# Kernel tuning notes

Measured on AMD Instinct MI355X. Metric: run time of the kernel, lower is better.

The kernel has to match this reference:

```python
import jax, jax.numpy as jnp
from jax import lax
import numpy as np

N = 2000      # num_nodes
T_IN = 24
T_OUT = 12
B = 32
H = 64        # hidden_dim
D = 10        # embed_dim / adapt_dim
K = 2         # cheb_k
C_IN = 1


def setup_inputs() -> dict:
    key = jax.random.key(0)
    ks = jax.random.split(key, 13)
    s = 0.1  # xavier-ish scale
    f32 = jnp.float32
    return {
        "x": jax.random.normal(ks[0], (B, T_IN, N), f32),
        "node_emb": jax.random.normal(ks[1], (N, D), f32) * s,
        "adapt_emb": jax.random.normal(ks[2], (N, D), f32) * s,
        # layer 0 NAPL weight/bias pools (gate: 2H out, candidate: H out)
        "Wg0": jax.random.normal(ks[3], (D, K, C_IN + H, 2 * H), f32) * s,
        "bg0": jax.random.normal(ks[4], (D, 2 * H), f32) * s,
        "Wc0": jax.random.normal(ks[5], (D, K, C_IN + H, H), f32) * s,
        "bc0": jax.random.normal(ks[6], (D, H), f32) * s,
        # layer 1 pools (input is hidden_dim)
        "Wg1": jax.random.normal(ks[7], (D, K, 2 * H, 2 * H), f32) * s,
        "bg1": jax.random.normal(ks[8], (D, 2 * H), f32) * s,
        "Wc1": jax.random.normal(ks[9], (D, K, 2 * H, H), f32) * s,
        "bc1": jax.random.normal(ks[10], (D, H), f32) * s,
        # 1x1 conv head == per-node linear hidden -> T_out
        "head_w": jax.random.normal(ks[11], (T_OUT, H), f32) * s,
        "head_b": jnp.zeros((T_OUT,), f32),
    }


def reference(x, node_emb, adapt_emb, Wg0, bg0, Wc0, bc0, Wg1, bg1, Wc1, bc1,
              head_w, head_b):
    Bn, T, Nn = x.shape
    # adaptive adjacency: row-softmax(relu(E E^T)); no prior -> A_used = A_adapt
    A = jax.nn.softmax(jax.nn.relu(adapt_emb @ adapt_emb.T), axis=-1)
    supports = jnp.stack([jnp.eye(Nn, dtype=x.dtype), A])  # (K, N, N)

    def napl(Wp, bp):
        # node-adaptive parameter learning: per-node weights/biases
        W = jnp.einsum('nd,dkio->nkio', node_emb, Wp)  # (N, K, Cin, Cout)
        b = node_emb @ bp                              # (N, Cout)
        return W, b

    p = [napl(Wg0, bg0), napl(Wc0, bc0), napl(Wg1, bg1), napl(Wc1, bc1)]

    def gconv(inp, W, b):
        # inp: (B, N, C)
        xg = jnp.einsum('knm,bmc->bknc', supports, inp)      # (B, K, N, C)
        return jnp.einsum('bkni,nkio->bno', xg, W) + b       # (B, N, Cout)

    def cell(xt, h, gW, gb, cW, cb):
        zr = jax.nn.sigmoid(gconv(jnp.concatenate([xt, h], -1), gW, gb))
        z, r = jnp.split(zr, 2, axis=-1)
        hc = jnp.tanh(gconv(jnp.concatenate([xt, r * h], -1), cW, cb))
        return z * h + (1.0 - z) * hc

    def step(carry, xt):
        h0, h1 = carry
        h0 = cell(xt, h0, p[0][0], p[0][1], p[1][0], p[1][1])
        h1 = cell(h0, h1, p[2][0], p[2][1], p[3][0], p[3][1])
        return (h0, h1), None

    xs = jnp.transpose(x[..., None], (1, 0, 2, 3))  # (T, B, N, 1)
    h0 = jnp.zeros((Bn, Nn, H), x.dtype)
    h1 = jnp.zeros((Bn, Nn, H), x.dtype)
    (h0, h1), _ = lax.scan(step, (h0, h1), xs)

    # 1x1 conv head on (B, H, N, 1) == per-node linear: (B, T_out, N)
    y = jnp.einsum('bnh,oh->bon', h1, head_w) + head_b[None, :, None]
    return y
```

## Files before the change

kernel.cpp:

```cpp
#include <hip/hip_runtime.h>
#include <math.h>

#define NN 2000
#define BB 32
#define TT 24
#define T_OUT 12
#define HH 64
#define DD 10
#define NP 2048
#define BC 2048

typedef unsigned short ushort_t;
typedef __bf16 bf16x8 __attribute__((ext_vector_type(8)));
typedef float f32x4 __attribute__((ext_vector_type(4)));

__device__ __forceinline__ float sigmoidf_(float x) { return 1.f / (1.f + expf(-x)); }

__device__ __forceinline__ ushort_t f2bf(float f) {
    unsigned int u = __float_as_uint(f);
    unsigned int r = (u + 0x7FFFu + ((u >> 16) & 1u)) >> 16;
    return (ushort_t)r;
}
__device__ __forceinline__ float bf2f(ushort_t s) {
    return __uint_as_float(((unsigned int)s) << 16);
}

__device__ __forceinline__ void glld16(const ushort_t* g, ushort_t* lds) {
    __builtin_amdgcn_global_load_lds(
        (const __attribute__((address_space(1))) char*)g,
        (__attribute__((address_space(3))) char*)lds, 16, 0, 0);
}

__device__ __forceinline__ unsigned lds_off(const void* p) {
    return (unsigned)(size_t)(__attribute__((address_space(3))) const char*)p;
}

constexpr size_t SZ_NPNP2 = (size_t)NP * NP * 2;
constexpr size_t SZ_ST4   = (size_t)NN * BC * 4;
constexpr size_t SZ_NPB2  = (size_t)NP * BC * 2;

constexpr size_t ABF_OFF  = 0;
constexpr size_t H0F_OFF  = ABF_OFF + SZ_NPNP2;
constexpr size_t H1F_OFF  = H0F_OFF + SZ_ST4;
constexpr size_t ZF_OFF   = H1F_OFF + SZ_ST4;
constexpr size_t H0B_OFF  = ZF_OFF + SZ_ST4;
constexpr size_t H1B_OFF  = H0B_OFF + SZ_NPB2;
constexpr size_t RHB_OFF  = H1B_OFF + SZ_NPB2;
constexpr size_t AH0_OFF  = RHB_OFF + SZ_NPB2;
constexpr size_t AHX_OFF  = AH0_OFF + SZ_NPB2;
constexpr size_t AXF_OFF  = AHX_OFF + SZ_NPB2;
constexpr size_t BTG0_OFF = AXF_OFF + (size_t)BB * TT * NN * 4;
constexpr size_t BTC0_OFF = BTG0_OFF + (size_t)DD * 128 * 128 * 2;
constexpr size_t BTG1_OFF = BTC0_OFF + (size_t)DD * 64 * 128 * 2;
constexpr size_t BTC1_OFF = BTG1_OFF + (size_t)DD * 128 * 256 * 2;
constexpr size_t WS_TOP   = BTC1_OFF + (size_t)DD * 64 * 256 * 2;

__global__ __launch_bounds__(256) void compute_A_kernel(const float* __restrict__ E,
                                                        float* __restrict__ A) {
    const int row = blockIdx.x;
    const int tid = threadIdx.x;
    float er[DD];
#pragma unroll
    for (int d = 0; d < DD; ++d) er[d] = E[row * DD + d];
    __shared__ float red[8];

    float lmax = -1e30f;
    for (int c = tid; c < NN; c += 256) {
        float s = 0.f;
#pragma unroll
        for (int d = 0; d < DD; ++d) s += er[d] * E[c * DD + d];
        s = fmaxf(s, 0.f);
        A[(size_t)row * NN + c] = s;
        lmax = fmaxf(lmax, s);
    }
#pragma unroll
    for (int o = 32; o > 0; o >>= 1) lmax = fmaxf(lmax, __shfl_down(lmax, o, 64));
    if ((tid & 63) == 0) red[tid >> 6] = lmax;
    __syncthreads();
    const float rmax = fmaxf(fmaxf(red[0], red[1]), fmaxf(red[2], red[3]));
    __syncthreads();

    float lsum = 0.f;
    for (int c = tid; c < NN; c += 256) {
        float v = expf(A[(size_t)row * NN + c] - rmax);
        A[(size_t)row * NN + c] = v;
        lsum += v;
    }
#pragma unroll
    for (int o = 32; o > 0; o >>= 1) lsum += __shfl_down(lsum, o, 64);
    if ((tid & 63) == 0) red[4 + (tid >> 6)] = lsum;
    __syncthreads();
    const float inv = 1.f / (red[4] + red[5] + red[6] + red[7]);
    for (int c = tid; c < NN; c += 256) A[(size_t)row * NN + c] *= inv;
}

__global__ __launch_bounds__(256) void convert_A(const float* __restrict__ Af,
                                                 ushort_t* __restrict__ Ab) {
    size_t idx = (size_t)blockIdx.x * 256 + threadIdx.x;
    int r = (int)(idx >> 11), c = (int)(idx & 2047);
    float v = (r < NN && c < NN) ? Af[(size_t)r * NN + c] : 0.f;
    Ab[idx] = f2bf(v);
}

__global__ __launch_bounds__(256) void ax_kernel(const float* __restrict__ A,
                                                 const float* __restrict__ x,
                                                 float* __restrict__ Ax) {
    __shared__ float As[64][65];
    __shared__ float xs[64][25];
    const int n0 = blockIdx.x * 64;
    const int b = blockIdx.y;
    const int tid = threadIdx.x;
    float acc[6] = {0, 0, 0, 0, 0, 0};
    for (int m0 = 0; m0 < NN; m0 += 64) {
#pragma unroll
        for (int l = 0; l < 16; ++l) {
            int idx = tid + l * 256;
            int r = idx >> 6, c = idx & 63;
            int n = n0 + r, m = m0 + c;
            As[r][c] = (n < NN && m < NN) ? A[(size_t)n * NN + m] : 0.f;
        }
        for (int idx = tid; idx < 64 * TT; idx += 256) {
            int c = idx >> 6, r = idx & 63;
            int m = m0 + r;
            xs[r][c] = (m < NN) ? x[((size_t)b * TT + c) * NN + m] : 0.f;
        }
        __syncthreads();
#pragma unroll 4
        for (int mm = 0; mm < 64; ++mm) {
#pragma unroll
            for (int j = 0; j < 6; ++j) {
                int oi = tid + j * 256;
                int r = oi / TT, c = oi % TT;
                acc[j] += As[r][mm] * xs[mm][c];
            }
        }
        __syncthreads();
    }
#pragma unroll
    for (int j = 0; j < 6; ++j) {
        int oi = tid + j * 256;
        int r = oi / TT, c = oi % TT;
        int n = n0 + r;
        if (n < NN) Ax[((size_t)b * TT + c) * NN + n] = acc[j];
    }
}

__global__ __launch_bounds__(256) void gemm_trb(const ushort_t* __restrict__ Ab,
                                                const ushort_t* __restrict__ H0,
                                                ushort_t* __restrict__ Y0,
                                                const ushort_t* __restrict__ H1,
                                                ushort_t* __restrict__ Y1) {
    __shared__ __align__(16) ushort_t As[64 * 32];
    __shared__ __align__(16) ushort_t Bs[32 * 128];
    const ushort_t* __restrict__ H = (blockIdx.z == 0) ? H0 : H1;
    ushort_t* __restrict__ Y = (blockIdx.z == 0) ? Y0 : Y1;
    const int tid = threadIdx.x;
    const int w = tid >> 6, l = tid & 63, lr = l & 15, lg = l >> 4;
    const int n0 = blockIdx.x * 64, j0 = blockIdx.y * 128;
    f32x4 acc[4][2] = {};

    const int arow = tid >> 2, ac16 = tid & 3;
    const size_t asrc = (size_t)(n0 + arow) * NP + ((ac16 ^ (arow & 3)) << 3);
    const unsigned bs0 = lds_off(Bs);
    const unsigned btr0 = bs0 + 2u * ((unsigned)(w * 2 + 0) * 512 + (unsigned)lg * 128 + (unsigned)lr);
    const unsigned btr1 = bs0 + 2u * ((unsigned)(w * 2 + 1) * 512 + (unsigned)lg * 128 + (unsigned)lr);

    for (int ks = 0; ks < NP / 32; ++ks) {
        const int m0 = ks * 32;
        glld16(Ab + asrc + m0, (ushort_t*)((char*)As + tid * 16));
#pragma unroll
        for (int p = 0; p < 2; ++p) {
            const int idx = p * 256 + tid;
            const int row = m0 + ((idx >> 3) & 7) * 4 + ((idx >> 1) & 3);
            const int col = j0 + (idx >> 6) * 16 + (idx & 1) * 8;
            glld16(H + (size_t)row * BC + col, (ushort_t*)((char*)Bs + idx * 16));
        }
        __syncthreads();

        bf16x8 av[4];
#pragma unroll
        for (int m = 0; m < 4; ++m) {
            const int rr = m * 16 + lr;
            av[m] = *(const bf16x8*)&As[rr * 32 + ((lg * 8) ^ ((rr & 3) << 3))];
        }
        unsigned long long bq0a, bq0b, bq1a, bq1b;
        asm volatile(
            "ds_read_b64_tr_b16 %0, %4 offset:0\n\t"
            "ds_read_b64_tr_b16 %1, %4 offset:128\n\t"
            "ds_read_b64_tr_b16 %2, %5 offset:0\n\t"
            "ds_read_b64_tr_b16 %3, %5 offset:128"
            : "=v"(bq0a), "=v"(bq0b), "=v"(bq1a), "=v"(bq1b)
            : "v"(btr0), "v"(btr1));
        asm volatile("s_waitcnt lgkmcnt(0)" ::: "memory");
        __builtin_amdgcn_sched_barrier(0);
        union { unsigned long long q[2]; bf16x8 f; } u0, u1;
        u0.q[0] = bq0a; u0.q[1] = bq0b;
        u1.q[0] = bq1a; u1.q[1] = bq1b;
        bf16x8 bv[2] = {u0.f, u1.f};

#pragma unroll
        for (int m = 0; m < 4; ++m)
#pragma unroll
            for (int nt = 0; nt < 2; ++nt)
                acc[m][nt] = __builtin_amdgcn_mfma_f32_16x16x32_bf16(av[m], bv[nt], acc[m][nt], 0, 0, 0);
        __syncthreads();
    }

#pragma unroll
    for (int m = 0; m < 4; ++m)
#pragma unroll
        for (int r = 0; r < 4; ++r) {
            const int n = n0 + m * 16 + lg * 4 + r;
            if (n < NN) {
#pragma unroll
                for (int nt = 0; nt < 2; ++nt)
                    Y[(size_t)n * BC + j0 + w * 32 + nt * 16 + lr] = f2bf(acc[m][nt][r]);
            }
        }
}

template <int CI, int CO, bool L0>
__global__ __launch_bounds__(256) void prepW(const float* __restrict__ Wp,
                                             ushort_t* __restrict__ Bt) {
    constexpr int K = L0 ? 128 : 256;
    const int idx = blockIdx.x * 256 + threadIdx.x;
    if (idx >= DD * CO * K) return;
    const int d = idx / (CO * K);
    const int rem = idx - d * CO * K;
    const int o = rem / K;
    const int k = rem - o * K;
    const int s = k >> 6, c = k & 63;
    const int kk = L0 ? s : (s & 1);
    const int i = L0 ? (1 + c) : ((s >> 1) * 64 + c);
    Bt[idx] = f2bf(Wp[((size_t)(d * 2 + kk) * CI + i) * CO + o]);
}

template <int NSEGS, int CO, bool GATE, bool HASX>
__global__ __launch_bounds__(256) void napl2(
    const ushort_t* __restrict__ Bt, const float* __restrict__ bp,
    const float* __restrict__ emb, const float* __restrict__ WxPool,
    const ushort_t* __restrict__ s0p, const ushort_t* __restrict__ s1p,
    const ushort_t* __restrict__ s2p, const ushort_t* __restrict__ s3p,
    const float* __restrict__ xv, const float* __restrict__ axv,
    const float* hf, float* __restrict__ zf,
    ushort_t* __restrict__ outb, float* outf, int t) {
    constexpr int K = NSEGS * 64;
    constexpr int NT = (CO == 128) ? 2 : 1;
    __shared__ __align__(16) ushort_t As[NSEGS * 64 * 64];
    const int tid = threadIdx.x;
    const int w = tid >> 6, l = tid & 63, lr = l & 15, lg = l >> 4;
    const int n0 = blockIdx.x * 2;
    const int ob = w * (16 * NT);
    const ushort_t* segs[4] = {s0p, s1p, s2p, s3p};

#pragma unroll
    for (int s = 0; s < NSEGS; ++s) {
        const ushort_t* sp = segs[s];
#pragma unroll
        for (int p = 0; p < 2; ++p) {
            const int idx = p * 256 + tid;
            const int row = idx >> 3, c16 = idx & 7;
            glld16(sp + (size_t)(n0 + (row >> 5)) * BC + (row & 31) * 64 +
                       ((c16 ^ (row & 7)) << 3),
                   (ushort_t*)((char*)As + s * 8192 + idx * 16));
        }
    }
    __syncthreads();

    f32x4 OUT[4][NT] = {};
#pragma unroll 1
    for (int d = 0; d < DD; ++d) {
        const ushort_t* btd = Bt + (size_t)d * CO * K;
        const float ea = emb[n0 * DD + d];
        const float eb = emb[(n0 + 1) * DD + d];
        f32x4 P[4][NT] = {};
#pragma unroll
        for (int s = 0; s < NSEGS; ++s)
#pragma unroll
            for (int h2 = 0; h2 < 2; ++h2) {
                const int kin = h2 * 32 + lg * 8;
                const int kg = s * 64 + kin;
                bf16x8 bv[NT];
#pragma unroll
                for (int nt = 0; nt < NT; ++nt)
                    bv[nt] = *(const bf16x8*)&btd[(size_t)(ob + nt * 16 + lr) * K + kg];
                bf16x8 av[4];
#pragma unroll
                for (int m = 0; m < 4; ++m) {
                    const int rr = m * 16 + lr;
                    av[m] = *(const bf16x8*)&As[s * 4096 + rr * 64 + (kin ^ ((rr & 7) << 3))];
                }
#pragma unroll
                for (int m = 0; m < 4; ++m)
#pragma unroll
                    for (int nt = 0; nt < NT; ++nt)
                        P[m][nt] = __builtin_amdgcn_mfma_f32_16x16x32_bf16(av[m], bv[nt], P[m][nt], 0, 0, 0);
            }
#pragma unroll
        for (int m = 0; m < 4; ++m) {
            const float e = (m < 2) ? ea : eb;
#pragma unroll
            for (int nt = 0; nt < NT; ++nt)
#pragma unroll
                for (int r = 0; r < 4; ++r)
                    OUT[m][nt][r] += e * P[m][nt][r];
        }
    }

    float bias[2][NT];
#pragma unroll
    for (int nd = 0; nd < 2; ++nd)
#pragma unroll
        for (int nt = 0; nt < NT; ++nt) {
            float s_ = 0.f;
#pragma unroll
            for (int d = 0; d < DD; ++d)
                s_ += emb[(n0 + nd) * DD + d] * bp[d * CO + ob + nt * 16 + lr];
            bias[nd][nt] = s_;
        }
    float wx[2][2][NT] = {};
    if (HASX) {
#pragma unroll
        for (int kk = 0; kk < 2; ++kk)
#pragma unroll
            for (int nd = 0; nd < 2; ++nd)
#pragma unroll
                for (int nt = 0; nt < NT; ++nt) {
                    float s_ = 0.f;
#pragma unroll
                    for (int d = 0; d < DD; ++d)
                        s_ += emb[(n0 + nd) * DD + d] *
                              WxPool[(size_t)(d * 2 + kk) * 65 * CO + ob + nt * 16 + lr];
                    wx[kk][nd][nt] = s_;
                }
    }

#pragma unroll
    for (int m = 0; m < 4; ++m) {
        const int nd = m >> 1;
        const int n = n0 + nd;
#pragma unroll
        for (int r = 0; r < 4; ++r) {
            const int row = m * 16 + lg * 4 + r;
            const int b = row & 31;
            const size_t nb = (size_t)n * BC + b * 64;
            float xt = 0.f, axt = 0.f;
            if (HASX) {
                xt = xv[((size_t)b * TT + t) * NN + n];
                axt = axv[((size_t)b * TT + t) * NN + n];
            }
#pragma unroll
            for (int nt = 0; nt < NT; ++nt) {
                const int o = ob + nt * 16 + lr;
                float val = OUT[m][nt][r] + bias[nd][nt];
                if (HASX) val += xt * wx[0][nd][nt] + axt * wx[1][nd][nt];
                if (GATE) {
                    const float sg = sigmoidf_(val);
                    if (ob < 64) {
                        zf[nb + o] = sg;
                    } else {
                        outb[nb + (o - 64)] = f2bf(sg * hf[nb + (o - 64)]);
                    }
                } else {
                    const float hc = tanhf(val);
                    const float z = zf[nb + o];
                    const float hn = z * hf[nb + o] + (1.f - z) * hc;
                    outf[nb + o] = hn;
                    outb[nb + o] = f2bf(hn);
                }
            }
        }
    }
}

__global__ __launch_bounds__(256) void head_kernel(const float* __restrict__ h1,
                                                   const float* __restrict__ hw,
                                                   const float* __restrict__ hb,
                                                   float* __restrict__ y) {
    __shared__ float wl[T_OUT * HH];
    const int tid = threadIdx.x;
    for (int idx = tid; idx < T_OUT * HH; idx += 256) wl[idx] = hw[idx];
    __syncthreads();
    const int gi = blockIdx.x * 256 + tid;
    if (gi >= BB * NN) return;
    const int b = gi / NN, n = gi % NN;
    float acc[T_OUT];
#pragma unroll
    for (int ot = 0; ot < T_OUT; ++ot) acc[ot] = hb[ot];
    for (int h = 0; h < HH; ++h) {
        float v = h1[(size_t)n * BC + b * 64 + h];
#pragma unroll
        for (int ot = 0; ot < T_OUT; ++ot) acc[ot] += v * wl[ot * HH + h];
    }
#pragma unroll
    for (int ot = 0; ot < T_OUT; ++ot)
        y[((size_t)b * T_OUT + ot) * NN + n] = acc[ot];
}

extern "C" void kernel_launch(void* const* d_in, const int* in_sizes, int n_in,
                              void* d_out, int out_size, void* d_ws, size_t ws_size,
                              hipStream_t stream) {
    const float* x = (const float*)d_in[0];
    const float* node_emb = (const float*)d_in[1];
    const float* adapt_emb = (const float*)d_in[2];
    const float* Wg0 = (const float*)d_in[3];
    const float* bg0 = (const float*)d_in[4];
    const float* Wc0 = (const float*)d_in[5];
    const float* bc0 = (const float*)d_in[6];
    const float* Wg1 = (const float*)d_in[7];
    const float* bg1 = (const float*)d_in[8];
    const float* Wc1 = (const float*)d_in[9];
    const float* bc1 = (const float*)d_in[10];
    const float* head_w = (const float*)d_in[11];
    const float* head_b = (const float*)d_in[12];
    float* y = (float*)d_out;

    char* ws = (char*)d_ws;
    ushort_t* Abf  = (ushort_t*)(ws + ABF_OFF);
    float* h0f = (float*)(ws + H0F_OFF);
    float* h1f = (float*)(ws + H1F_OFF);
    float* zf  = (float*)(ws + ZF_OFF);
    ushort_t* h0b = (ushort_t*)(ws + H0B_OFF);
    ushort_t* h1b = (ushort_t*)(ws + H1B_OFF);
    ushort_t* rhb = (ushort_t*)(ws + RHB_OFF);
    ushort_t* Ah0 = (ushort_t*)(ws + AH0_OFF);
    ushort_t* AhX = (ushort_t*)(ws + AHX_OFF);
    float* Axf = (float*)(ws + AXF_OFF);
    ushort_t* Btg0 = (ushort_t*)(ws + BTG0_OFF);
    ushort_t* Btc0 = (ushort_t*)(ws + BTC0_OFF);
    ushort_t* Btg1 = (ushort_t*)(ws + BTG1_OFF);
    ushort_t* Btc1 = (ushort_t*)(ws + BTC1_OFF);
    float* Af32 = zf;

    hipMemsetAsync(h0f, 0, SZ_ST4, stream);
    hipMemsetAsync(h1f, 0, SZ_ST4, stream);
    hipMemsetAsync(h0b, 0, SZ_NPB2, stream);
    hipMemsetAsync(h1b, 0, SZ_NPB2, stream);
    hipMemsetAsync(rhb, 0, SZ_NPB2, stream);
    hipMemsetAsync(Ah0, 0, SZ_NPB2, stream);
    hipMemsetAsync(AhX, 0, SZ_NPB2, stream);

    compute_A_kernel<<<NN, 256, 0, stream>>>(adapt_emb, Af32);
    ax_kernel<<<dim3((NN + 63) / 64, BB), 256, 0, stream>>>(Af32, x, Axf);
    convert_A<<<(NP * NP) / 256, 256, 0, stream>>>(Af32, Abf);
    prepW<65, 128, true><<<(DD * 128 * 128 + 255) / 256, 256, 0, stream>>>(Wg0, Btg0);
    prepW<65, 64, true><<<(DD * 64 * 128 + 255) / 256, 256, 0, stream>>>(Wc0, Btc0);
    prepW<128, 128, false><<<(DD * 128 * 256 + 255) / 256, 256, 0, stream>>>(Wg1, Btg1);
    prepW<128, 64, false><<<(DD * 64 * 256 + 255) / 256, 256, 0, stream>>>(Wc1, Btc1);

    const dim3 gG1(NP / 64, NP / 128, 1);
    const dim3 gG2(NP / 64, NP / 128, 2);
    const int gN = NN * BB / 64;

    for (int t = 0; t < TT; ++t) {
        napl2<2, 128, true, true><<<gN, 256, 0, stream>>>(
            Btg0, bg0, node_emb, Wg0, h0b, Ah0, h0b, h0b, x, Axf, h0f, zf, rhb, nullptr, t);
        gemm_trb<<<gG1, 256, 0, stream>>>(Abf, rhb, AhX, rhb, AhX);
        napl2<2, 64, false, true><<<gN, 256, 0, stream>>>(
            Btc0, bc0, node_emb, Wc0, rhb, AhX, rhb, rhb, x, Axf, h0f, zf, h0b, h0f, t);
        gemm_trb<<<gG2, 256, 0, stream>>>(Abf, h0b, Ah0, h1b, AhX);
        napl2<4, 128, true, false><<<gN, 256, 0, stream>>>(
            Btg1, bg1, node_emb, nullptr, h0b, Ah0, h1b, AhX, nullptr, nullptr, h1f, zf, rhb, nullptr, t);
        gemm_trb<<<gG1, 256, 0, stream>>>(Abf, rhb, AhX, rhb, AhX);
        napl2<4, 64, false, false><<<gN, 256, 0, stream>>>(
            Btc1, bc1, node_emb, nullptr, h0b, Ah0, rhb, AhX, nullptr, nullptr, h1f, zf, h1b, h1f, t);
    }

    head_kernel<<<(BB * NN + 255) / 256, 256, 0, stream>>>(h1f, head_w, head_b, y);
}
```

Before: 9.788 ms.

## Register-tile the A·x precompute kernel across four batches per block

Replaces the A·x precompute kernel with a version in which each block covers 64 nodes for 4 batches at once, so each A tile is loaded once per four batches instead of once per batch. The tile is stored transposed in shared memory and each thread computes a 4x6 register tile using vectorized shared loads, replacing the per-element integer div/mod indexing. This cuts global reads of A and shared-memory traffic in a one-time setup kernel, at the cost of more shared memory and registers per block and a grid of only 256 blocks.

```diff
diff --git a/kernel.cpp b/kernel.cpp
--- a/kernel.cpp
+++ b/kernel.cpp
@@ -102,46 +102,60 @@
     Ab[idx] = f2bf(v);
 }
 
-__global__ __launch_bounds__(256) void ax_kernel(const float* __restrict__ A,
-                                                 const float* __restrict__ x,
-                                                 float* __restrict__ Ax) {
-    __shared__ float As[64][65];
-    __shared__ float xs[64][25];
+__global__ __launch_bounds__(256) void ax2_kernel(const float* __restrict__ A,
+                                                  const float* __restrict__ x,
+                                                  float* __restrict__ Ax) {
+    __shared__ float As[64][68];
+    __shared__ float xs[64][98];
     const int n0 = blockIdx.x * 64;
-    const int b = blockIdx.y;
+    const int b0 = blockIdx.y * 4;
     const int tid = threadIdx.x;
-    float acc[6] = {0, 0, 0, 0, 0, 0};
+    const int tr = tid >> 4, tc = tid & 15;
+    float acc[4][6] = {};
+
     for (int m0 = 0; m0 < NN; m0 += 64) {
 #pragma unroll
         for (int l = 0; l < 16; ++l) {
             int idx = tid + l * 256;
-            int r = idx >> 6, c = idx & 63;
-            int n = n0 + r, m = m0 + c;
-            As[r][c] = (n < NN && m < NN) ? A[(size_t)n * NN + m] : 0.f;
-        }
-        for (int idx = tid; idx < 64 * TT; idx += 256) {
-            int c = idx >> 6, r = idx & 63;
-            int m = m0 + r;
-            xs[r][c] = (m < NN) ? x[((size_t)b * TT + c) * NN + m] : 0.f;
+            int mm = idx & 63, r = idx >> 6;
+            int n = n0 + r, m = m0 + mm;
+            As[mm][r] = (n < NN && m < NN) ? A[(size_t)n * NN + m] : 0.f;
+        }
+#pragma unroll
+        for (int l = 0; l < 24; ++l) {
+            int idx = tid + l * 256;
+            int mm = idx & 63, col = idx >> 6;
+            int m = m0 + mm;
+            int bl = col / 24, t = col - bl * 24;
+            xs[mm][col] = (m < NN) ? x[((size_t)(b0 + bl) * TT + t) * NN + m] : 0.f;
         }
         __syncthreads();
 #pragma unroll 4
         for (int mm = 0; mm < 64; ++mm) {
+            float4 a4 = *(const float4*)&As[mm][tr * 4];
+            float xv[6];
+            *(float2*)&xv[0] = *(const float2*)&xs[mm][tc * 6];
+            *(float2*)&xv[2] = *(const float2*)&xs[mm][tc * 6 + 2];
+            *(float2*)&xv[4] = *(const float2*)&xs[mm][tc * 6 + 4];
+            float av[4] = {a4.x, a4.y, a4.z, a4.w};
+#pragma unroll
+            for (int i = 0; i < 4; ++i)
+#pragma unroll
+                for (int j = 0; j < 6; ++j) acc[i][j] += av[i] * xv[j];
+        }
+        __syncthreads();
+    }
+#pragma unroll
+    for (int i = 0; i < 4; ++i) {
+        const int n = n0 + tr * 4 + i;
+        if (n < NN) {
 #pragma unroll
             for (int j = 0; j < 6; ++j) {
-                int oi = tid + j * 256;
-                int r = oi / TT, c = oi % TT;
-                acc[j] += As[r][mm] * xs[mm][c];
+                int col = tc * 6 + j;
+                int bl = col / 24, t = col - bl * 24;
+                Ax[((size_t)(b0 + bl) * TT + t) * NN + n] = acc[i][j];
             }
         }
-        __syncthreads();
-    }
-#pragma unroll
-    for (int j = 0; j < 6; ++j) {
-        int oi = tid + j * 256;
-        int r = oi / TT, c = oi % TT;
-        int n = n0 + r;
-        if (n < NN) Ax[((size_t)b * TT + c) * NN + n] = acc[j];
     }
 }
 
@@ -441,7 +455,7 @@
     hipMemsetAsync(AhX, 0, SZ_NPB2, stream);
 
     compute_A_kernel<<<NN, 256, 0, stream>>>(adapt_emb, Af32);
-    ax_kernel<<<dim3((NN + 63) / 64, BB), 256, 0, stream>>>(Af32, x, Axf);
+    ax2_kernel<<<dim3(32, 8), 256, 0, stream>>>(Af32, x, Axf);
     convert_A<<<(NP * NP) / 256, 256, 0, stream>>>(Af32, Abf);
     prepW<65, 128, true><<<(DD * 128 * 128 + 255) / 256, 256, 0, stream>>>(Wg0, Btg0);
     prepW<65, 64, true><<<(DD * 64 * 128 + 255) / 256, 256, 0, stream>>>(Wc0, Btc0);
```

Measured after the change: 9.729 ms. Within noise of the previous version (-0.6%).
